# Optimization experiments

Measured on AMD Instinct MI355X. Metric: run time of the kernel, lower is better.

## Reference

```python
import jax, jax.numpy as jnp
import numpy as np

K = 8          # num groups
SIZE = 250     # state/hidden size (h1 = h2 = 250)
M = 576        # flattened input size (24x24)
B = 2048       # batch
HA = 100       # attention hidden
EPS = 1e-5


def _ln(x, g, b):
    mu = jnp.mean(x, axis=-1, keepdims=True)
    v = jnp.mean(jnp.square(x - mu), axis=-1, keepdims=True)
    return (x - mu) * jax.lax.rsqrt(v + EPS) * g + b


def setup_inputs() -> dict:
    key = jax.random.key(0)
    ks = jax.random.split(key, 10)
    def w(k, shape):
        return jax.random.normal(k, shape, jnp.float32) / np.sqrt(shape[0]).astype(np.float32)
    inp = {
        "x": jax.random.normal(ks[0], (B * K, M), jnp.float32),
        "state": jax.random.normal(ks[1], (B * K, SIZE), jnp.float32),
        # encoder: Linear(SIZE,250) + ReLU + LN(250)
        "enc_W": w(ks[2], (SIZE, 250)), "enc_b": jnp.zeros((250,), jnp.float32),
        "enc_g": jnp.ones((250,), jnp.float32), "enc_bt": jnp.zeros((250,), jnp.float32),
        # core: Linear(500,250) + ReLU + LN(250)
        "core_W": w(ks[3], (500, 250)), "core_b": jnp.zeros((250,), jnp.float32),
        "core_g": jnp.ones((250,), jnp.float32), "core_bt": jnp.zeros((250,), jnp.float32),
        # context: Linear(250,250) + ReLU + LN(250)
        "ctx_W": w(ks[4], (250, 250)), "ctx_b": jnp.zeros((250,), jnp.float32),
        "ctx_g": jnp.ones((250,), jnp.float32), "ctx_bt": jnp.zeros((250,), jnp.float32),
        # attention: Linear(250,100)+Tanh+LN(100)+Linear(100,1)+Sigmoid
        "att_W1": w(ks[5], (250, HA)), "att_b1": jnp.zeros((HA,), jnp.float32),
        "att_g": jnp.ones((HA,), jnp.float32), "att_bt": jnp.zeros((HA,), jnp.float32),
        "att_W2": w(ks[6], (HA, 1)), "att_b2": jnp.zeros((1,), jnp.float32),
        # output: Linear(250 + 250 + M, SIZE)
        "out_W": w(ks[7], (250 + 250 + M, SIZE)), "out_b": jnp.zeros((SIZE,), jnp.float32),
    }
    return inp


def reference(x, state, enc_W, enc_b, enc_g, enc_bt, core_W, core_b, core_g, core_bt,
              ctx_W, ctx_b, ctx_g, ctx_bt, att_W1, att_b1, att_g, att_bt,
              att_W2, att_b2, out_W, out_b):
    bk = state.shape[0]
    b = bk // K
    h1 = 250
    # 0-1. encode state -> [B*K, h1]
    s1 = _ln(jax.nn.relu(state @ enc_W + enc_b), enc_g, enc_bt)
    s1r = s1.reshape(b, K, h1)
    # 2-3. focus / context pairs via static gather index [K, K-1]
    idx = np.array([[j for j in range(K) if j != i] for i in range(K)], np.int32)
    cs = s1r[:, idx]                                    # [b, K, K-1, h1]
    fs = jnp.broadcast_to(s1r[:, :, None, :], cs.shape)  # [b, K, K-1, h1]
    # 4. concat pairs -> [b*K*(K-1), 2*h1]
    concat = jnp.concatenate([fs, cs], axis=-1).reshape(b * K * (K - 1), 2 * h1)
    # 5. core MLP
    core_out = _ln(jax.nn.relu(concat @ core_W + core_b), core_g, core_bt)
    # context MLP
    context_out = _ln(jax.nn.relu(core_out @ ctx_W + ctx_b), ctx_g, ctx_bt)
    # attention scalar per pair
    att_h = _ln(jnp.tanh(core_out @ att_W1 + att_b1), att_g, att_bt)
    att = jax.nn.sigmoid(att_h @ att_W2 + att_b2)        # [b*K*(K-1), 1]
    # 6-7. attention-weighted sum over K-1 context effects -> [B*K, h2]
    effect_sum = jnp.sum(context_out.reshape(bk, K - 1, h1) * att.reshape(bk, K - 1, 1), axis=1)
    # 8. decode
    total = jnp.concatenate([s1, effect_sum, x], axis=1)  # [B*K, h1+h2+M]
    new_state = total @ out_W + out_b                     # [B*K, SIZE]
    return new_state
```

## Files before the change

kernel.cpp:

```cpp
#include <hip/hip_runtime.h>
#include <math.h>

#define KK 8
#define H 250
#define MDIM 576
#define NB 2048
#define HA 100
#define ROWS (NB*KK)
#define PROWS (ROWS*7)
#define PQS 512
#define KP 1088
#define CSLD 352
#define EPS 1e-5f

typedef unsigned short ushort_t;
typedef short short8 __attribute__((ext_vector_type(8)));
typedef unsigned short us8 __attribute__((ext_vector_type(8)));
typedef unsigned short us4 __attribute__((ext_vector_type(4)));
typedef unsigned short us2 __attribute__((ext_vector_type(2)));
typedef float f32x4 __attribute__((ext_vector_type(4)));

template<int CTRL>
__device__ __forceinline__ float dpp_add_f32(float x) {
    const int s = __builtin_amdgcn_update_dpp(
        0, __builtin_bit_cast(int, x), CTRL, 0xF, 0xF, true);
    return x + __builtin_bit_cast(float, s);
}
__device__ __forceinline__ float wave_sum_dpp(float x) {
    x = dpp_add_f32<0x111>(x);
    x = dpp_add_f32<0x112>(x);
    x = dpp_add_f32<0x114>(x);
    x = dpp_add_f32<0x118>(x);
    x = dpp_add_f32<0x142>(x);
    x = dpp_add_f32<0x143>(x);
    return __builtin_bit_cast(float, __builtin_amdgcn_readlane(
        __builtin_bit_cast(int, x), 63));
}

__device__ __forceinline__ void async_copy16(const void* g, void* l) {
    __builtin_amdgcn_global_load_lds(
        (const __attribute__((address_space(1))) void*)g,
        (__attribute__((address_space(3))) void*)l, 16, 0, 0);
}

__device__ __forceinline__ ushort_t f2bf(float v) {
    union { float f; unsigned int u; } c; c.f = v;
    unsigned int x = c.u;
    x += 0x7fff + ((x >> 16) & 1);
    return (ushort_t)(x >> 16);
}
__device__ __forceinline__ float bf2f(ushort_t v) {
    union { unsigned int u; float f; } c; c.u = ((unsigned int)v) << 16;
    return c.f;
}
__device__ __forceinline__ float ftanh(float x) {
    const float e = __expf(2.f * x);
    return 1.f - 2.f * __builtin_amdgcn_rcpf(e + 1.f);
}
__device__ __forceinline__ float fsigmoid(float x) {
    return __builtin_amdgcn_rcpf(1.f + __expf(-x));
}

__global__ __launch_bounds__(256) void k_prep(
    const float* __restrict__ out_W, const float* __restrict__ core_W,
    const float* __restrict__ ctx_W, const float* __restrict__ att_W1,
    const float* __restrict__ enc_W, const float* __restrict__ state,
    const float* __restrict__ x,
    ushort_t* __restrict__ Wt, ushort_t* __restrict__ Wpq,
    ushort_t* __restrict__ Wca, ushort_t* __restrict__ Wenc,
    ushort_t* __restrict__ Sb, ushort_t* __restrict__ Abuf)
{
    const int b = blockIdx.x, t = threadIdx.x;
    if (b < 256) {
        const int n = b;
        for (int k = t; k < KP; k += 256) {
            const float v = (n < H && k < 1076) ? out_W[(size_t)k * H + n] : 0.f;
            Wt[(size_t)n * KP + k] = f2bf(v);
        }
    } else if (b < 768) {
        const int n = b - 256, k = t;
        float v = 0.f;
        if (k < H) {
            if (n < H)                    v = core_W[(size_t)k * H + n];
            else if (n >= 256 && n < 506) v = core_W[(size_t)(H + k) * H + (n - 256)];
        }
        Wpq[(size_t)n * 256 + k] = f2bf(v);
    } else if (b < 1152) {
        const int n = b - 768, k = t;
        float v = 0.f;
        if (k < H) {
            if (n < H)           v = ctx_W[(size_t)k * H + n];
            else if (n < H + HA) v = att_W1[(size_t)k * HA + (n - H)];
        }
        Wca[(size_t)n * 256 + k] = f2bf(v);
    } else if (b < 1408) {
        const int n = b - 1152, k = t;
        const float v = (n < H && k < H) ? enc_W[(size_t)k * H + n] : 0.f;
        Wenc[(size_t)n * 256 + k] = f2bf(v);
    } else if (b < 2432) {
        const int r0 = (b - 1408) * 16;
        for (int idx = t; idx < 16 * 256; idx += 256) {
            const int r = r0 + (idx >> 8), k = idx & 255;
            const float v = (k < H) ? state[(size_t)r * H + k] : 0.f;
            Sb[(size_t)r * 256 + k] = f2bf(v);
        }
    } else {
        const int row = b - 2432;
        for (int c = 500 + t; c < KP; c += 256) {
            const float v = (c < 500 + MDIM) ? x[(size_t)row * MDIM + (c - 500)] : 0.f;
            Abuf[(size_t)row * KP + c] = f2bf(v);
        }
    }
}

template<int NT>
__global__ __launch_bounds__(512, NT == 8 ? 2 : 4) void k_gemm_nres(
    const ushort_t* __restrict__ A, int lda,
    const ushort_t* __restrict__ B, int ldb,
    void* __restrict__ Cp, int ldc,
    const float* __restrict__ bias,
    int ksteps, int nlim, int bf16out)
{
    constexpr int NROWS = NT * 64;
    __shared__ __align__(16) ushort_t As[64 * 32];
    __shared__ __align__(16) ushort_t Bs[NROWS * 32];
    const int tid = threadIdx.x, lane = tid & 63, wave = tid >> 6;
    const int wm = wave >> 2, wn = wave & 3;
    const int R0 = (int)blockIdx.x * 64;

    const int ar = tid >> 2, acb = tid & 3;
    const bool aon = tid < 256;
    const int acl = acb ^ ((ar >> 1) & 3);
    const ushort_t* gA = A + (size_t)(R0 + ar) * lda + acl * 8;

    const int q = lane >> 4, fr = lane & 15;

    f32x4 acc[2][NT] = {};
    for (int ks = 0; ks < ksteps; ++ks) {
        const int k0 = ks * 32;
        if (aon) async_copy16(gA + k0, &As[tid * 8]);
#pragma unroll
        for (int it = 0; it < NT / 2; ++it) {
            const int ci  = it * 512 + tid;
            const int rb  = ci >> 2, cb2 = ci & 3;
            const int clb = cb2 ^ ((rb >> 1) & 3);
            async_copy16(B + (size_t)rb * ldb + k0 + clb * 8, &Bs[ci * 8]);
        }
        __syncthreads();
        short8 a[2];
#pragma unroll
        for (int ms = 0; ms < 2; ++ms) {
            const int row = wm * 32 + ms * 16 + fr;
            a[ms] = *(const short8*)&As[(row * 4 + (q ^ ((row >> 1) & 3))) * 8];
        }
#pragma unroll
        for (int nt = 0; nt < NT; ++nt) {
            const int n = wn * (NT * 16) + nt * 16 + fr;
            const short8 b = *(const short8*)&Bs[(n * 4 + (q ^ ((n >> 1) & 3))) * 8];
#pragma unroll
            for (int ms = 0; ms < 2; ++ms)
                acc[ms][nt] = __builtin_amdgcn_mfma_f32_16x16x32_bf16(
                    a[ms], b, acc[ms][nt], 0, 0, 0);
        }
        __syncthreads();
    }

#pragma unroll
    for (int ms = 0; ms < 2; ++ms)
#pragma unroll
        for (int nt = 0; nt < NT; ++nt) {
            const int col = wn * (NT * 16) + nt * 16 + fr;
            if (col >= nlim) continue;
            const float bv = bias ? bias[col] : 0.f;
#pragma unroll
            for (int reg = 0; reg < 4; ++reg) {
                const int row = R0 + wm * 32 + ms * 16 + q * 4 + reg;
                const float v = acc[ms][nt][reg] + bv;
                if (bf16out) ((ushort_t*)Cp)[(size_t)row * ldc + col] = f2bf(v);
                else         ((float*)Cp)[(size_t)row * ldc + col] = v;
            }
        }
}

__global__ __launch_bounds__(256) void k_lnenc(const ushort_t* __restrict__ Epre,
    const float* __restrict__ eb, const float* __restrict__ eg,
    const float* __restrict__ ebt, ushort_t* __restrict__ Abuf)
{
    const int wave = threadIdx.x >> 6, lane = threadIdx.x & 63;
    const int row = blockIdx.x * 4 + wave;
    const int c0 = 4 * lane;

    const us4 v = *(const us4*)&Epre[(size_t)row * 256 + c0];
    float y[4]; float sm = 0.f, sq = 0.f;
#pragma unroll
    for (int t = 0; t < 4; ++t) {
        const int cc = c0 + t;
        float z = 0.f;
        if (cc < H) z = fmaxf(bf2f(v[t]) + eb[cc], 0.f);
        y[t] = z; sm += z; sq += z * z;
    }
    sm = wave_sum_dpp(sm);
    sq = wave_sum_dpp(sq);
    const float mu = sm * (1.f / H);
    const float rs = __builtin_amdgcn_rsqf(sq * (1.f / H) - mu * mu + EPS);
    ushort_t o[4];
#pragma unroll
    for (int t = 0; t < 4; ++t) {
        const int cc = c0 + t;
        o[t] = (cc < H) ? f2bf((y[t] - mu) * rs * eg[cc] + ebt[cc]) : (ushort_t)0;
    }
    ushort_t* dst = Abuf + (size_t)row * KP + c0;
    if (c0 + 3 < H) { *(us4*)dst = (us4){o[0], o[1], o[2], o[3]}; }
    else {
        if (c0 + 1 < H) *(us2*)dst = (us2){o[0], o[1]};
    }
}

__global__ __launch_bounds__(256) void k_core(const ushort_t* __restrict__ PQb,
    const float* __restrict__ core_b, const float* __restrict__ core_g,
    const float* __restrict__ core_bt, ushort_t* __restrict__ Co)
{
    const int wave = threadIdx.x >> 6, lane = threadIdx.x & 63;
    const int g = blockIdx.x * 4 + wave;
    const int i = g & 7;
    const int c = lane * 4;

    const us4 pu = *(const us4*)&PQb[(size_t)g * PQS + c];
    us4 qu[7];
#pragma unroll
    for (int jj = 0; jj < 7; ++jj) {
        const int j = jj + (jj >= i ? 1 : 0);
        const int qr = (g & ~7) + j;
        qu[jj] = *(const us4*)&PQb[(size_t)qr * PQS + 256 + c];
    }
    float pe[4], cb[4], cg[4], cbt[4]; bool vl[4];
#pragma unroll
    for (int t = 0; t < 4; ++t) {
        vl[t]  = (c + t) < H;
        pe[t]  = bf2f(pu[t]);
        cb[t]  = vl[t] ? core_b[c + t]  : 0.f;
        cg[t]  = vl[t] ? core_g[c + t]  : 0.f;
        cbt[t] = vl[t] ? core_bt[c + t] : 0.f;
    }
    float z[7][4], red[7][2];
#pragma unroll
    for (int jj = 0; jj < 7; ++jj) {
        float sm = 0.f, sq = 0.f;
#pragma unroll
        for (int t = 0; t < 4; ++t) {
            const float zz = vl[t] ? fmaxf(pe[t] + bf2f(qu[jj][t]) + cb[t], 0.f) : 0.f;
            z[jj][t] = zz; sm += zz; sq = fmaf(zz, zz, sq);
        }
        red[jj][0] = sm; red[jj][1] = sq;
    }
#pragma unroll
    for (int jj = 0; jj < 7; ++jj) {
        red[jj][0] = wave_sum_dpp(red[jj][0]);
        red[jj][1] = wave_sum_dpp(red[jj][1]);
    }
#pragma unroll
    for (int jj = 0; jj < 7; ++jj) {
        const float mu = red[jj][0] * (1.f / H);
        const float rs = __builtin_amdgcn_rsqf(red[jj][1] * (1.f / H) - mu * mu + EPS);
        us4 o;
#pragma unroll
        for (int t = 0; t < 4; ++t)
            o[t] = vl[t] ? f2bf((z[jj][t] - mu) * rs * cg[t] + cbt[t]) : (ushort_t)0;
        *(us4*)&Co[((size_t)g * 7 + jj) * 256 + c] = o;
    }
}

__global__ __launch_bounds__(512, 4) void k_cs(
    const ushort_t* __restrict__ Co,
    const ushort_t* __restrict__ Wca,
    ushort_t* __restrict__ Cs)
{
    __shared__ __align__(16) ushort_t As[64 * 32];
    __shared__ __align__(16) ushort_t Bs[384 * 32];
    const int tid = threadIdx.x, lane = tid & 63, wave = tid >> 6;
    const int wm = wave >> 2, wn = wave & 3;
    const int R0 = (int)blockIdx.x * 64;

    const int ar = tid >> 2, acb = tid & 3;
    const bool aon = tid < 256;
    const int acl = acb ^ ((ar >> 1) & 3);
    const ushort_t* gA = Co + (size_t)(R0 + ar) * 256 + acl * 8;

    const int q = lane >> 4, fr = lane & 15;

    f32x4 acc[2][6] = {};
    for (int ks = 0; ks < 8; ++ks) {
        const int k0 = ks * 32;
        if (aon) async_copy16(gA + k0, &As[tid * 8]);
#pragma unroll
        for (int it = 0; it < 3; ++it) {
            const int ci  = it * 512 + tid;
            const int rb  = ci >> 2, cb2 = ci & 3;
            const int clb = cb2 ^ ((rb >> 1) & 3);
            async_copy16(Wca + (size_t)rb * 256 + k0 + clb * 8, &Bs[ci * 8]);
        }
        __syncthreads();
        short8 a[2];
#pragma unroll
        for (int ms = 0; ms < 2; ++ms) {
            const int row = wm * 32 + ms * 16 + fr;
            a[ms] = *(const short8*)&As[(row * 4 + (q ^ ((row >> 1) & 3))) * 8];
        }
#pragma unroll
        for (int nt = 0; nt < 6; ++nt) {
            const int n = wn * 96 + nt * 16 + fr;
            const short8 b = *(const short8*)&Bs[(n * 4 + (q ^ ((n >> 1) & 3))) * 8];
#pragma unroll
            for (int ms = 0; ms < 2; ++ms)
                acc[ms][nt] = __builtin_amdgcn_mfma_f32_16x16x32_bf16(
                    a[ms], b, acc[ms][nt], 0, 0, 0);
        }
        __syncthreads();
    }

#pragma unroll
    for (int ms = 0; ms < 2; ++ms)
#pragma unroll
        for (int nt = 0; nt < 6; ++nt) {
            const int col = wn * 96 + nt * 16 + fr;
            if (col >= CSLD) continue;
#pragma unroll
            for (int reg = 0; reg < 4; ++reg) {
                const int row = R0 + wm * 32 + ms * 16 + q * 4 + reg;
                Cs[(size_t)row * CSLD + col] = f2bf(acc[ms][nt][reg]);
            }
        }
}

__global__ __launch_bounds__(256) void k_eff(const ushort_t* __restrict__ Cs,
    const float* __restrict__ ctx_b, const float* __restrict__ ctx_g, const float* __restrict__ ctx_bt,
    const float* __restrict__ att_b1, const float* __restrict__ att_g, const float* __restrict__ att_bt,
    const float* __restrict__ attW2, const float* __restrict__ att_b2,
    ushort_t* __restrict__ Abuf)
{
    const int wave = threadIdx.x >> 6, lane = threadIdx.x & 63;
    const int g = blockIdx.x * 4 + wave;
    const int c0 = 4 * lane;
    const int c1 = 256 + 2 * lane;
    const bool l48 = lane < 48;

    int ce[6]; bool eC[6], eA[6]; float b_[6], g_[6], bt_[6], w2_[6], gw[6];
#pragma unroll
    for (int e = 0; e < 6; ++e) {
        ce[e] = (e < 4) ? (c0 + e) : (c1 + (e - 4));
        const bool vld = (e < 4) || l48;
        eC[e] = vld && (ce[e] < H);
        eA[e] = vld && (ce[e] >= H) && (ce[e] < H + HA);
        if (eC[e])      { b_[e] = ctx_b[ce[e]]; g_[e] = ctx_g[ce[e]]; bt_[e] = ctx_bt[ce[e]]; w2_[e] = 0.f; }
        else if (eA[e]) { const int ca = ce[e] - H;
                          b_[e] = att_b1[ca]; g_[e] = att_g[ca]; bt_[e] = att_bt[ca]; w2_[e] = attW2[ca]; }
        else            { b_[e] = g_[e] = bt_[e] = w2_[e] = 0.f; }
        gw[e] = eA[e] ? g_[e] * w2_[e] : 0.f;
    }
    float sgw = 0.f, sbw = 0.f;
#pragma unroll
    for (int e = 0; e < 6; ++e) if (eA[e]) {
        sgw += g_[e] * w2_[e];
        sbw += bt_[e] * w2_[e];
    }
    sgw = wave_sum_dpp(sgw);
    sbw = wave_sum_dpp(sbw);
    const float ab2 = att_b2[0] + sbw;

    us4 v0[7]; us2 v1[7];
#pragma unroll
    for (int jj = 0; jj < 7; ++jj) {
        const size_t base = ((size_t)g * 7 + jj) * CSLD;
        v0[jj] = *(const us4*)&Cs[base + c0];
        v1[jj] = l48 ? *(const us2*)&Cs[base + c1] : (us2){0, 0};
    }

    float z[7][4], red[7][5];
#pragma unroll
    for (int jj = 0; jj < 7; ++jj) {
        float smc = 0.f, sqc = 0.f, sma = 0.f, sqa = 0.f, szgw = 0.f;
#pragma unroll
        for (int e = 0; e < 6; ++e) {
            const float raw = (e < 4) ? bf2f(v0[jj][e]) : bf2f(v1[jj][e - 4]);
            float zz = 0.f;
            if (eC[e]) {
                zz = fmaxf(raw + b_[e], 0.f);
                smc += zz; sqc = fmaf(zz, zz, sqc);
            } else if (eA[e]) {
                const float za = ftanh(raw + b_[e]);
                sma += za; sqa = fmaf(za, za, sqa);
                szgw = fmaf(za, gw[e], szgw);
            }
            if (e < 4) z[jj][e] = zz;
        }
        red[jj][0] = smc; red[jj][1] = sqc; red[jj][2] = sma;
        red[jj][3] = sqa; red[jj][4] = szgw;
    }

#pragma unroll
    for (int jj = 0; jj < 7; ++jj)
#pragma unroll
        for (int v = 0; v < 5; ++v)
            red[jj][v] = wave_sum_dpp(red[jj][v]);

    float A4[4] = {0.f, 0.f, 0.f, 0.f};
    float S0 = 0.f, S1 = 0.f;
#pragma unroll
    for (int jj = 0; jj < 7; ++jj) {
        const float muC = red[jj][0] * (1.f / H);
        const float rsC = __builtin_amdgcn_rsqf(red[jj][1] * (1.f / H) - muC * muC + EPS);
        const float muA = red[jj][2] * (1.f / HA);
        const float rsA = __builtin_amdgcn_rsqf(red[jj][3] * (1.f / HA) - muA * muA + EPS);
        const float dot = rsA * (red[jj][4] - muA * sgw) + ab2;
        const float ag  = fsigmoid(dot);
        const float cj  = ag * rsC;
        S0 += ag; S1 = fmaf(cj, muC, S1);
#pragma unroll
        for (int e = 0; e < 4; ++e) A4[e] = fmaf(cj, z[jj][e], A4[e]);
    }
    ushort_t o[4];
#pragma unroll
    for (int e = 0; e < 4; ++e)
        o[e] = f2bf(g_[e] * (A4[e] - S1) + bt_[e] * S0);
    ushort_t* dst = Abuf + (size_t)g * KP + H + c0;
    if (c0 + 1 < H) *(us2*)dst       = (us2){o[0], o[1]};
    if (c0 + 3 < H) *(us2*)(dst + 2) = (us2){o[2], o[3]};
}

extern "C" void kernel_launch(void* const* d_in, const int* in_sizes, int n_in,
                              void* d_out, int out_size, void* d_ws, size_t ws_size,
                              hipStream_t stream)
{
    const float* x      = (const float*)d_in[0];
    const float* state  = (const float*)d_in[1];
    const float* enc_W  = (const float*)d_in[2];
    const float* enc_b  = (const float*)d_in[3];
    const float* enc_g  = (const float*)d_in[4];
    const float* enc_bt = (const float*)d_in[5];
    const float* core_W = (const float*)d_in[6];
    const float* core_b = (const float*)d_in[7];
    const float* core_g = (const float*)d_in[8];
    const float* core_bt= (const float*)d_in[9];
    const float* ctx_W  = (const float*)d_in[10];
    const float* ctx_b  = (const float*)d_in[11];
    const float* ctx_g  = (const float*)d_in[12];
    const float* ctx_bt = (const float*)d_in[13];
    const float* att_W1 = (const float*)d_in[14];
    const float* att_b1 = (const float*)d_in[15];
    const float* att_g  = (const float*)d_in[16];
    const float* att_bt = (const float*)d_in[17];
    const float* att_W2 = (const float*)d_in[18];
    const float* att_b2 = (const float*)d_in[19];
    const float* out_W  = (const float*)d_in[20];
    const float* out_b  = (const float*)d_in[21];
    float* out = (float*)d_out;

    ushort_t* Abuf = (ushort_t*)d_ws;
    ushort_t* Wt   = Abuf + (size_t)ROWS * KP;
    ushort_t* Wpq  = Wt + (size_t)256 * KP;
    ushort_t* Wca  = Wpq + (size_t)512 * 256;
    ushort_t* Wenc = Wca + (size_t)384 * 256;
    ushort_t* Co   = Wenc + (size_t)256 * 256;
    ushort_t* Cs   = Co + (size_t)PROWS * 256;
    ushort_t* Sb   = Cs;
    ushort_t* Epre = Sb + (size_t)ROWS * 256;
    ushort_t* PQb  = Epre + (size_t)ROWS * 256;

    k_prep  <<<2432 + ROWS, 256, 0, stream>>>(out_W, core_W, ctx_W, att_W1, enc_W,
                                              state, x, Wt, Wpq, Wca, Wenc, Sb, Abuf);
    k_gemm_nres<4><<<ROWS / 64, 512, 0, stream>>>(Sb, 256, Wenc, 256, Epre, 256,
                                                  nullptr, 8, 256, 1);
    k_lnenc <<<ROWS / 4, 256, 0, stream>>>(Epre, enc_b, enc_g, enc_bt, Abuf);
    k_gemm_nres<8><<<ROWS / 64, 512, 0, stream>>>(Abuf, KP, Wpq, 256, PQb, PQS,
                                                  nullptr, 8, 512, 1);
    k_core  <<<ROWS / 4, 256, 0, stream>>>(PQb, core_b, core_g, core_bt, Co);
    k_cs    <<<PROWS / 64, 512, 0, stream>>>(Co, Wca, Cs);
    k_eff   <<<ROWS / 4, 256, 0, stream>>>(Cs, ctx_b, ctx_g, ctx_bt,
                                           att_b1, att_g, att_bt, att_W2, att_b2,
                                           Abuf);
    k_gemm_nres<4><<<ROWS / 64, 512, 0, stream>>>(Abuf, KP, Wt, KP, out, H,
                                                  out_b, KP / 32, 250, 0);
}
```

Baseline: 324.8 us.

## Fuse core LN, context/attention GEMM and effect reduction into one kernel

```diff
diff --git a/kernel.cpp b/kernel.cpp
--- a/kernel.cpp
+++ b/kernel.cpp
@@ -7,10 +7,8 @@
 #define NB 2048
 #define HA 100
 #define ROWS (NB*KK)
-#define PROWS (ROWS*7)
 #define PQS 512
 #define KP 1088
-#define CSLD 352
 #define EPS 1e-5f
 
 typedef unsigned short ushort_t;
@@ -35,6 +33,13 @@
     x = dpp_add_f32<0x143>(x);
     return __builtin_bit_cast(float, __builtin_amdgcn_readlane(
         __builtin_bit_cast(int, x), 63));
+}
+__device__ __forceinline__ float bfly16_sum(float x) {
+    x = dpp_add_f32<0xB1>(x);
+    x = dpp_add_f32<0x4E>(x);
+    x = dpp_add_f32<0x141>(x);
+    x = dpp_add_f32<0x140>(x);
+    return x;
 }
 
 __device__ __forceinline__ void async_copy16(const void* g, void* l) {
@@ -216,215 +221,206 @@
     }
 }
 
-__global__ __launch_bounds__(256) void k_core(const ushort_t* __restrict__ PQb,
+__global__ __launch_bounds__(512, 4) void k_fuse(
+    const ushort_t* __restrict__ PQb,
+    const ushort_t* __restrict__ Wca,
     const float* __restrict__ core_b, const float* __restrict__ core_g,
-    const float* __restrict__ core_bt, ushort_t* __restrict__ Co)
-{
-    const int wave = threadIdx.x >> 6, lane = threadIdx.x & 63;
-    const int g = blockIdx.x * 4 + wave;
-    const int i = g & 7;
-    const int c = lane * 4;
-
-    const us4 pu = *(const us4*)&PQb[(size_t)g * PQS + c];
-    us4 qu[7];
-#pragma unroll
-    for (int jj = 0; jj < 7; ++jj) {
-        const int j = jj + (jj >= i ? 1 : 0);
-        const int qr = (g & ~7) + j;
-        qu[jj] = *(const us4*)&PQb[(size_t)qr * PQS + 256 + c];
-    }
-    float pe[4], cb[4], cg[4], cbt[4]; bool vl[4];
-#pragma unroll
-    for (int t = 0; t < 4; ++t) {
-        vl[t]  = (c + t) < H;
-        pe[t]  = bf2f(pu[t]);
-        cb[t]  = vl[t] ? core_b[c + t]  : 0.f;
-        cg[t]  = vl[t] ? core_g[c + t]  : 0.f;
-        cbt[t] = vl[t] ? core_bt[c + t] : 0.f;
-    }
-    float z[7][4], red[7][2];
-#pragma unroll
-    for (int jj = 0; jj < 7; ++jj) {
-        float sm = 0.f, sq = 0.f;
-#pragma unroll
-        for (int t = 0; t < 4; ++t) {
-            const float zz = vl[t] ? fmaxf(pe[t] + bf2f(qu[jj][t]) + cb[t], 0.f) : 0.f;
-            z[jj][t] = zz; sm += zz; sq = fmaf(zz, zz, sq);
-        }
-        red[jj][0] = sm; red[jj][1] = sq;
-    }
-#pragma unroll
-    for (int jj = 0; jj < 7; ++jj) {
-        red[jj][0] = wave_sum_dpp(red[jj][0]);
-        red[jj][1] = wave_sum_dpp(red[jj][1]);
-    }
-#pragma unroll
-    for (int jj = 0; jj < 7; ++jj) {
-        const float mu = red[jj][0] * (1.f / H);
-        const float rs = __builtin_amdgcn_rsqf(red[jj][1] * (1.f / H) - mu * mu + EPS);
-        us4 o;
-#pragma unroll
-        for (int t = 0; t < 4; ++t)
-            o[t] = vl[t] ? f2bf((z[jj][t] - mu) * rs * cg[t] + cbt[t]) : (ushort_t)0;
-        *(us4*)&Co[((size_t)g * 7 + jj) * 256 + c] = o;
-    }
-}
-
-__global__ __launch_bounds__(512, 4) void k_cs(
-    const ushort_t* __restrict__ Co,
-    const ushort_t* __restrict__ Wca,
-    ushort_t* __restrict__ Cs)
-{
-    __shared__ __align__(16) ushort_t As[64 * 32];
-    __shared__ __align__(16) ushort_t Bs[384 * 32];
-    const int tid = threadIdx.x, lane = tid & 63, wave = tid >> 6;
-    const int wm = wave >> 2, wn = wave & 3;
-    const int R0 = (int)blockIdx.x * 64;
-
-    const int ar = tid >> 2, acb = tid & 3;
-    const bool aon = tid < 256;
-    const int acl = acb ^ ((ar >> 1) & 3);
-    const ushort_t* gA = Co + (size_t)(R0 + ar) * 256 + acl * 8;
-
-    const int q = lane >> 4, fr = lane & 15;
-
-    f32x4 acc[2][6] = {};
-    for (int ks = 0; ks < 8; ++ks) {
-        const int k0 = ks * 32;
-        if (aon) async_copy16(gA + k0, &As[tid * 8]);
-#pragma unroll
-        for (int it = 0; it < 3; ++it) {
-            const int ci  = it * 512 + tid;
-            const int rb  = ci >> 2, cb2 = ci & 3;
-            const int clb = cb2 ^ ((rb >> 1) & 3);
-            async_copy16(Wca + (size_t)rb * 256 + k0 + clb * 8, &Bs[ci * 8]);
-        }
-        __syncthreads();
-        short8 a[2];
-#pragma unroll
-        for (int ms = 0; ms < 2; ++ms) {
-            const int row = wm * 32 + ms * 16 + fr;
-            a[ms] = *(const short8*)&As[(row * 4 + (q ^ ((row >> 1) & 3))) * 8];
-        }
-#pragma unroll
-        for (int nt = 0; nt < 6; ++nt) {
-            const int n = wn * 96 + nt * 16 + fr;
-            const short8 b = *(const short8*)&Bs[(n * 4 + (q ^ ((n >> 1) & 3))) * 8];
-#pragma unroll
-            for (int ms = 0; ms < 2; ++ms)
-                acc[ms][nt] = __builtin_amdgcn_mfma_f32_16x16x32_bf16(
-                    a[ms], b, acc[ms][nt], 0, 0, 0);
-        }
-        __syncthreads();
-    }
-
-#pragma unroll
-    for (int ms = 0; ms < 2; ++ms)
-#pragma unroll
-        for (int nt = 0; nt < 6; ++nt) {
-            const int col = wn * 96 + nt * 16 + fr;
-            if (col >= CSLD) continue;
-#pragma unroll
-            for (int reg = 0; reg < 4; ++reg) {
-                const int row = R0 + wm * 32 + ms * 16 + q * 4 + reg;
-                Cs[(size_t)row * CSLD + col] = f2bf(acc[ms][nt][reg]);
-            }
-        }
-}
-
-__global__ __launch_bounds__(256) void k_eff(const ushort_t* __restrict__ Cs,
-    const float* __restrict__ ctx_b, const float* __restrict__ ctx_g, const float* __restrict__ ctx_bt,
-    const float* __restrict__ att_b1, const float* __restrict__ att_g, const float* __restrict__ att_bt,
+    const float* __restrict__ core_bt,
+    const float* __restrict__ ctx_b, const float* __restrict__ ctx_g,
+    const float* __restrict__ ctx_bt,
+    const float* __restrict__ att_b1, const float* __restrict__ att_g,
+    const float* __restrict__ att_bt,
     const float* __restrict__ attW2, const float* __restrict__ att_b2,
     ushort_t* __restrict__ Abuf)
 {
-    const int wave = threadIdx.x >> 6, lane = threadIdx.x & 63;
-    const int g = blockIdx.x * 4 + wave;
-    const int c0 = 4 * lane;
-    const int c1 = 256 + 2 * lane;
-    const bool l48 = lane < 48;
-
-    int ce[6]; bool eC[6], eA[6]; float b_[6], g_[6], bt_[6], w2_[6], gw[6];
-#pragma unroll
-    for (int e = 0; e < 6; ++e) {
-        ce[e] = (e < 4) ? (c0 + e) : (c1 + (e - 4));
-        const bool vld = (e < 4) || l48;
-        eC[e] = vld && (ce[e] < H);
-        eA[e] = vld && (ce[e] >= H) && (ce[e] < H + HA);
-        if (eC[e])      { b_[e] = ctx_b[ce[e]]; g_[e] = ctx_g[ce[e]]; bt_[e] = ctx_bt[ce[e]]; w2_[e] = 0.f; }
-        else if (eA[e]) { const int ca = ce[e] - H;
-                          b_[e] = att_b1[ca]; g_[e] = att_g[ca]; bt_[e] = att_bt[ca]; w2_[e] = attW2[ca]; }
-        else            { b_[e] = g_[e] = bt_[e] = w2_[e] = 0.f; }
-        gw[e] = eA[e] ? g_[e] * w2_[e] : 0.f;
-    }
-    float sgw = 0.f, sbw = 0.f;
-#pragma unroll
-    for (int e = 0; e < 6; ++e) if (eA[e]) {
-        sgw += g_[e] * w2_[e];
-        sbw += bt_[e] * w2_[e];
-    }
-    sgw = wave_sum_dpp(sgw);
-    sbw = wave_sum_dpp(sbw);
-    const float ab2 = att_b2[0] + sbw;
-
-    us4 v0[7]; us2 v1[7];
-#pragma unroll
+    __shared__ __align__(16) ushort_t As[32 * 256];
+    __shared__ __align__(16) ushort_t Bs[384 * 32];
+    __shared__ __align__(16) float red[32][36];
+    __shared__ __align__(16) float scal[32][4];
+    __shared__ float swred[4][2];
+
+    const int tid = threadIdx.x, lane = tid & 63, wave = tid >> 6;
+    const int wm = wave >> 2, wn = wave & 3;
+    const int q = lane >> 4, fr = lane & 15;
+    const int g0 = (int)blockIdx.x * 32;
+
+    bool eC[6], eA[6];
+    float b_[6], g_[6], bt_[6], gw[6];
+    float psgw = 0.f, psbw = 0.f;
+#pragma unroll
+    for (int nt = 0; nt < 6; ++nt) {
+        const int col = wn * 96 + nt * 16 + fr;
+        eC[nt] = col < H;
+        eA[nt] = (col >= H) && (col < H + HA);
+        if (eC[nt]) {
+            b_[nt] = ctx_b[col]; g_[nt] = ctx_g[col]; bt_[nt] = ctx_bt[col]; gw[nt] = 0.f;
+        } else if (eA[nt]) {
+            const int ca = col - H;
+            b_[nt] = att_b1[ca]; g_[nt] = att_g[ca]; bt_[nt] = att_bt[ca];
+            const float w2 = attW2[ca];
+            gw[nt] = g_[nt] * w2;
+            psgw += gw[nt]; psbw += bt_[nt] * w2;
+        } else {
+            b_[nt] = g_[nt] = bt_[nt] = gw[nt] = 0.f;
+        }
+    }
+    psgw = bfly16_sum(psgw); psbw = bfly16_sum(psbw);
+    if (lane == 0) { swred[wn][0] = psgw; swred[wn][1] = psbw; }
+    __syncthreads();
+    const float sgw = swred[0][0] + swred[1][0] + swred[2][0] + swred[3][0];
+    const float ab2 = att_b2[0] +
+        (swred[0][1] + swred[1][1] + swred[2][1] + swred[3][1]);
+
+    const int cL = lane * 4;
+    float cb4[4], cg4[4], cbt4[4]; bool vl4[4];
+#pragma unroll
+    for (int t = 0; t < 4; ++t) {
+        vl4[t] = (cL + t) < H;
+        cb4[t] = cg4[t] = cbt4[t] = 0.f;
+        if (vl4[t]) { cb4[t] = core_b[cL + t]; cg4[t] = core_g[cL + t];
+                      cbt4[t] = core_bt[cL + t]; }
+    }
+    us4 puR[4];
+#pragma unroll
+    for (int pass = 0; pass < 4; ++pass) {
+        const int r = pass * 8 + wave;
+        puR[pass] = *(const us4*)&PQb[(size_t)(g0 + r) * PQS + cL];
+    }
+    const int pSlot = (((lane >> 1) ^ 0) << 1) | (lane & 1);
+    (void)pSlot;
+
+    const int arow = wm * 16 + fr;
+    const int abase = arow * 256;
+    const int arsw = arow & 7;
+
+    f32x4 A4[6] = {};
+    float S0[4] = {0.f, 0.f, 0.f, 0.f}, S1[4] = {0.f, 0.f, 0.f, 0.f};
+
     for (int jj = 0; jj < 7; ++jj) {
-        const size_t base = ((size_t)g * 7 + jj) * CSLD;
-        v0[jj] = *(const us4*)&Cs[base + c0];
-        v1[jj] = l48 ? *(const us2*)&Cs[base + c1] : (us2){0, 0};
-    }
-
-    float z[7][4], red[7][5];
-#pragma unroll
-    for (int jj = 0; jj < 7; ++jj) {
-        float smc = 0.f, sqc = 0.f, sma = 0.f, sqa = 0.f, szgw = 0.f;
-#pragma unroll
-        for (int e = 0; e < 6; ++e) {
-            const float raw = (e < 4) ? bf2f(v0[jj][e]) : bf2f(v1[jj][e - 4]);
-            float zz = 0.f;
-            if (eC[e]) {
-                zz = fmaxf(raw + b_[e], 0.f);
-                smc += zz; sqc = fmaf(zz, zz, sqc);
-            } else if (eA[e]) {
-                const float za = ftanh(raw + b_[e]);
-                sma += za; sqa = fmaf(za, za, sqa);
-                szgw = fmaf(za, gw[e], szgw);
-            }
-            if (e < 4) z[jj][e] = zz;
-        }
-        red[jj][0] = smc; red[jj][1] = sqc; red[jj][2] = sma;
-        red[jj][3] = sqa; red[jj][4] = szgw;
-    }
-
-#pragma unroll
-    for (int jj = 0; jj < 7; ++jj)
-#pragma unroll
-        for (int v = 0; v < 5; ++v)
-            red[jj][v] = wave_sum_dpp(red[jj][v]);
-
-    float A4[4] = {0.f, 0.f, 0.f, 0.f};
-    float S0 = 0.f, S1 = 0.f;
-#pragma unroll
-    for (int jj = 0; jj < 7; ++jj) {
-        const float muC = red[jj][0] * (1.f / H);
-        const float rsC = __builtin_amdgcn_rsqf(red[jj][1] * (1.f / H) - muC * muC + EPS);
-        const float muA = red[jj][2] * (1.f / HA);
-        const float rsA = __builtin_amdgcn_rsqf(red[jj][3] * (1.f / HA) - muA * muA + EPS);
-        const float dot = rsA * (red[jj][4] - muA * sgw) + ab2;
-        const float ag  = fsigmoid(dot);
-        const float cj  = ag * rsC;
-        S0 += ag; S1 = fmaf(cj, muC, S1);
-#pragma unroll
-        for (int e = 0; e < 4; ++e) A4[e] = fmaf(cj, z[jj][e], A4[e]);
-    }
-    ushort_t o[4];
-#pragma unroll
-    for (int e = 0; e < 4; ++e)
-        o[e] = f2bf(g_[e] * (A4[e] - S1) + bt_[e] * S0);
-    ushort_t* dst = Abuf + (size_t)g * KP + H + c0;
-    if (c0 + 1 < H) *(us2*)dst       = (us2){o[0], o[1]};
-    if (c0 + 3 < H) *(us2*)(dst + 2) = (us2){o[2], o[3]};
+#pragma unroll
+        for (int pass = 0; pass < 4; ++pass) {
+            const int r = pass * 8 + wave;
+            const int ir = r & 7;
+            const int j = jj + (jj >= ir ? 1 : 0);
+            const us4 qu = *(const us4*)&PQb[
+                (size_t)(g0 + (r & ~7) + j) * PQS + 256 + cL];
+            const us4 pu = puR[pass];
+            float z[4]; float sm = 0.f, sq = 0.f;
+#pragma unroll
+            for (int t = 0; t < 4; ++t) {
+                float zz = 0.f;
+                if (vl4[t]) zz = fmaxf(bf2f(pu[t]) + bf2f(qu[t]) + cb4[t], 0.f);
+                z[t] = zz; sm += zz; sq = fmaf(zz, zz, sq);
+            }
+            sm = wave_sum_dpp(sm);
+            sq = wave_sum_dpp(sq);
+            const float mu = sm * (1.f / H);
+            const float rs = __builtin_amdgcn_rsqf(sq * (1.f / H) - mu * mu + EPS);
+            us4 o;
+#pragma unroll
+            for (int t = 0; t < 4; ++t)
+                o[t] = vl4[t] ? f2bf((z[t] - mu) * rs * cg4[t] + cbt4[t])
+                              : (ushort_t)0;
+            const int p = (((lane >> 1) ^ (r & 7)) << 1) | (lane & 1);
+            *(us4*)&As[r * 256 + p * 4] = o;
+        }
+
+        f32x4 acc[6] = {};
+        for (int ks = 0; ks < 8; ++ks) {
+#pragma unroll
+            for (int it = 0; it < 3; ++it) {
+                const int ci  = it * 512 + tid;
+                const int rb  = ci >> 2, cb2 = ci & 3;
+                const int clb = cb2 ^ ((rb >> 1) & 3);
+                async_copy16(Wca + (size_t)rb * 256 + ks * 32 + clb * 8, &Bs[ci * 8]);
+            }
+            __syncthreads();
+            const short8 a = *(const short8*)&As[abase + ((ks * 4 + q) ^ arsw) * 8];
+#pragma unroll
+            for (int nt = 0; nt < 6; ++nt) {
+                const int n = wn * 96 + nt * 16 + fr;
+                const short8 b = *(const short8*)&Bs[(n * 4 + (q ^ ((n >> 1) & 3))) * 8];
+                acc[nt] = __builtin_amdgcn_mfma_f32_16x16x32_bf16(a, b, acc[nt], 0, 0, 0);
+            }
+            __syncthreads();
+        }
+
+        float smc[4] = {}, sqc[4] = {}, sma[4] = {}, sqa[4] = {}, szgw[4] = {};
+#pragma unroll
+        for (int nt = 0; nt < 6; ++nt) {
+#pragma unroll
+            for (int reg = 0; reg < 4; ++reg) {
+                const float val = acc[nt][reg] + b_[nt];
+                if (eC[nt]) {
+                    const float zz = fmaxf(val, 0.f);
+                    acc[nt][reg] = zz;
+                    smc[reg] += zz; sqc[reg] = fmaf(zz, zz, sqc[reg]);
+                } else if (eA[nt]) {
+                    const float za = ftanh(val);
+                    sma[reg] += za; sqa[reg] = fmaf(za, za, sqa[reg]);
+                    szgw[reg] = fmaf(za, gw[nt], szgw[reg]);
+                }
+            }
+        }
+#pragma unroll
+        for (int reg = 0; reg < 4; ++reg) {
+            smc[reg]  = bfly16_sum(smc[reg]);
+            sqc[reg]  = bfly16_sum(sqc[reg]);
+            sma[reg]  = bfly16_sum(sma[reg]);
+            sqa[reg]  = bfly16_sum(sqa[reg]);
+            szgw[reg] = bfly16_sum(szgw[reg]);
+        }
+        if (fr == 0) {
+#pragma unroll
+            for (int reg = 0; reg < 4; ++reg) {
+                const int row = wm * 16 + q * 4 + reg;
+                *(f32x4*)&red[row][wn * 8] =
+                    (f32x4){smc[reg], sqc[reg], sma[reg], sqa[reg]};
+                red[row][wn * 8 + 4] = szgw[reg];
+            }
+        }
+        __syncthreads();
+        if (wave == 0 && lane < 32) {
+            const int rr = lane;
+            float s0 = 0.f, s1 = 0.f, s2 = 0.f, s3 = 0.f, s4 = 0.f;
+#pragma unroll
+            for (int w2 = 0; w2 < 4; ++w2) {
+                const f32x4 v = *(const f32x4*)&red[rr][w2 * 8];
+                s0 += v[0]; s1 += v[1]; s2 += v[2]; s3 += v[3];
+                s4 += red[rr][w2 * 8 + 4];
+            }
+            const float muC = s0 * (1.f / H);
+            const float rsC = __builtin_amdgcn_rsqf(s1 * (1.f / H) - muC * muC + EPS);
+            const float muA = s2 * (1.f / HA);
+            const float rsA = __builtin_amdgcn_rsqf(s3 * (1.f / HA) - muA * muA + EPS);
+            const float dot = rsA * (s4 - muA * sgw) + ab2;
+            const float ag  = fsigmoid(dot);
+            const float cj  = ag * rsC;
+            *(f32x4*)&scal[rr][0] = (f32x4){cj, ag, cj * muC, 0.f};
+        }
+        __syncthreads();
+#pragma unroll
+        for (int reg = 0; reg < 4; ++reg) {
+            const int row = wm * 16 + q * 4 + reg;
+            const f32x4 sc = *(const f32x4*)&scal[row][0];
+            S0[reg] += sc[1]; S1[reg] += sc[2];
+#pragma unroll
+            for (int nt = 0; nt < 6; ++nt)
+                A4[nt][reg] = fmaf(sc[0], acc[nt][reg], A4[nt][reg]);
+        }
+    }
+
+#pragma unroll
+    for (int nt = 0; nt < 6; ++nt) {
+        const int col = wn * 96 + nt * 16 + fr;
+        if (col >= H) continue;
+#pragma unroll
+        for (int reg = 0; reg < 4; ++reg) {
+            const int row = wm * 16 + q * 4 + reg;
+            const float o = g_[nt] * (A4[nt][reg] - S1[reg]) + bt_[nt] * S0[reg];
+            Abuf[(size_t)(g0 + row) * KP + H + col] = f2bf(o);
+        }
+    }
 }
 
 extern "C" void kernel_launch(void* const* d_in, const int* in_sizes, int n_in,
@@ -460,9 +456,7 @@
     ushort_t* Wpq  = Wt + (size_t)256 * KP;
     ushort_t* Wca  = Wpq + (size_t)512 * 256;
     ushort_t* Wenc = Wca + (size_t)384 * 256;
-    ushort_t* Co   = Wenc + (size_t)256 * 256;
-    ushort_t* Cs   = Co + (size_t)PROWS * 256;
-    ushort_t* Sb   = Cs;
+    ushort_t* Sb   = Wenc + (size_t)256 * 256;
     ushort_t* Epre = Sb + (size_t)ROWS * 256;
     ushort_t* PQb  = Epre + (size_t)ROWS * 256;
 
@@ -473,11 +467,11 @@
     k_lnenc <<<ROWS / 4, 256, 0, stream>>>(Epre, enc_b, enc_g, enc_bt, Abuf);
     k_gemm_nres<8><<<ROWS / 64, 512, 0, stream>>>(Abuf, KP, Wpq, 256, PQb, PQS,
                                                   nullptr, 8, 512, 1);
-    k_core  <<<ROWS / 4, 256, 0, stream>>>(PQb, core_b, core_g, core_bt, Co);
-    k_cs    <<<PROWS / 64, 512, 0, stream>>>(Co, Wca, Cs);
-    k_eff   <<<ROWS / 4, 256, 0, stream>>>(Cs, ctx_b, ctx_g, ctx_bt,
-                                           att_b1, att_g, att_bt, att_W2, att_b2,
-                                           Abuf);
+    k_fuse  <<<ROWS / 32, 512, 0, stream>>>(PQb, Wca,
+                                            core_b, core_g, core_bt,
+                                            ctx_b, ctx_g, ctx_bt,
+                                            att_b1, att_g, att_bt,
+                                            att_W2, att_b2, Abuf);
     k_gemm_nres<4><<<ROWS / 64, 512, 0, stream>>>(Abuf, KP, Wt, KP, out, H,
                                                   out_b, KP / 32, 250, 0);
 }
```

After: 466.0 us. 43.5% more time.
